# Optimization experiments

Hardware: AMD Instinct MI355X
Metric: run time of the kernel (lower is better)

The kernel has to match this reference:

```python
import jax, jax.numpy as jnp
import numpy as np

B, N, D = 2, 2048, 768
H = 12
DH = D // H
SCALE = DH ** -0.5


def setup_inputs() -> dict:
    key = jax.random.key(0)
    k1, k2, k3 = jax.random.split(key, 3)
    x = jax.random.normal(k1, (B, N, D), dtype=jnp.float32)
    w_qkv = jax.random.normal(k2, (D, 3 * D), dtype=jnp.float32) * (D ** -0.5)
    b_qkv = jnp.zeros((3 * D,), dtype=jnp.float32)
    w_proj = jax.random.normal(k3, (D, D), dtype=jnp.float32) * (D ** -0.5)
    b_proj = jnp.zeros((D,), dtype=jnp.float32)
    return {"x": x, "w_qkv": w_qkv, "b_qkv": b_qkv, "w_proj": w_proj, "b_proj": b_proj}


def reference(x, w_qkv, b_qkv, w_proj, b_proj):
    b, n, d = x.shape
    # qkv: (B, n, 3, H, DH) -> (3, B, H, n, DH)
    qkv = (x @ w_qkv + b_qkv).reshape(b, n, 3, H, DH).transpose(2, 0, 3, 1, 4)
    q, k, v = qkv[0], qkv[1], qkv[2]
    # naive full attention matrix (B, H, n, n)
    attn = jnp.einsum('bhqd,bhkd->bhqk', q, k) * SCALE
    attn = jax.nn.softmax(attn, axis=-1)
    out = jnp.einsum('bhqk,bhkd->bhqd', attn, v)  # (B, H, n, DH)
    out = out.transpose(0, 2, 1, 3).reshape(b, n, d)
    return out @ w_proj + b_proj
```

## Files before the change

kernel.cpp:

```cpp
#include <hip/hip_runtime.h>


#define CB 2
#define CN 2048
#define CD 768
#define CH 12
#define CDH 64
#define CEXPSCALE 0.18033688f

typedef __bf16 bf16x8 __attribute__((ext_vector_type(8)));
typedef float f32x4 __attribute__((ext_vector_type(4)));
typedef unsigned short u16x8 __attribute__((ext_vector_type(8)));

static __device__ __forceinline__ unsigned short f2bf(float f) {
  union { float f; unsigned u; } v; v.f = f;
  unsigned r = v.u + 0x7fffu + ((v.u >> 16) & 1u);
  return (unsigned short)(r >> 16);
}

static __device__ __forceinline__ void gld_lds16(const unsigned short* g, unsigned short* lds_base) {
  __builtin_amdgcn_global_load_lds(
      (const __attribute__((address_space(1))) unsigned int*)g,
      (__attribute__((address_space(3))) unsigned int*)(unsigned int)(unsigned long long)lds_base,
      16, 0, 0);
}

__global__ __launch_bounds__(256) void prep(const float* __restrict__ x,
                                            unsigned short* __restrict__ xb,
                                            const float* __restrict__ w_qkv,
                                            unsigned short* __restrict__ wqkv_t,
                                            const float* __restrict__ w_proj,
                                            unsigned short* __restrict__ wproj_t) {
  __shared__ __align__(16) unsigned short t[64][72];
  const int bid = blockIdx.x, tid = threadIdx.x;
#pragma unroll
  for (int it = 0; it < 2; ++it) {
    size_t i = ((size_t)(bid * 2 + it) * 256 + tid) * 8;
    f32x4 a = *(const f32x4*)&x[i];
    f32x4 b = *(const f32x4*)&x[i + 4];
    u16x8 o;
#pragma unroll
    for (int j = 0; j < 4; ++j) { o[j] = f2bf(a[j]); o[4 + j] = f2bf(b[j]); }
    *(u16x8*)&xb[i] = o;
  }
  if (bid >= 576) return;
  const float* src; unsigned short* dst; int R, C, c0, r0;
  if (bid < 432) { src = w_qkv; dst = wqkv_t; R = 768; C = 2304; c0 = (bid % 36) * 64; r0 = (bid / 36) * 64; }
  else { int u = bid - 432; src = w_proj; dst = wproj_t; R = 768; C = 768; c0 = (u % 12) * 64; r0 = (u / 12) * 64; }
#pragma unroll
  for (int i = 0; i < 4; ++i) {
    int c = tid + i * 256;
    int row = c >> 4, cc = (c & 15) * 4;
    f32x4 v = *(const f32x4*)&src[(size_t)(r0 + row) * C + c0 + cc];
#pragma unroll
    for (int j = 0; j < 4; ++j) t[row][cc + j] = f2bf(v[j]);
  }
  __syncthreads();
#pragma unroll
  for (int i = 0; i < 2; ++i) {
    int c = tid + i * 256;
    int drow = c >> 3, rc = (c & 7) * 8;
    u16x8 v;
#pragma unroll
    for (int j = 0; j < 8; ++j) v[j] = t[rc + j][drow];
    *(u16x8*)&dst[(size_t)(c0 + drow) * R + r0 + rc] = v;
  }
}

extern __shared__ __align__(16) unsigned short smem[];

template <int TM, int TN>
__global__ __launch_bounds__(256, 4) void gemm_db(const unsigned short* __restrict__ A,
                                                  const unsigned short* __restrict__ Bt,
                                                  const float* __restrict__ bias,
                                                  int M, int N, int K, int mode,
                                                  unsigned short* __restrict__ o0,
                                                  unsigned short* __restrict__ o1,
                                                  unsigned short* __restrict__ o2,
                                                  float* __restrict__ outF) {
  constexpr int NT = TN / 32;
  unsigned short* As = smem;
  unsigned short* Bs = smem + 2 * TM * 32;
  unsigned short* Ct = smem;
  const int tid = threadIdx.x;
  const int w = tid >> 6, lane = tid & 63, quad = lane >> 4, lc = lane & 15;
  const int wm = (w >> 1) * 32, wn = (w & 1) * (TN / 2);
  const int row0 = blockIdx.y * TM, col0 = blockIdx.x * TN;
  f32x4 acc[2][NT] = {};

  const int rl = lane >> 2, cl = lane & 3;
  const int gc = cl ^ ((rl >> 1) & 3);
  const int rsw = (lc >> 1) & 3;
  const int nk = K / 32;

  auto stage = [&](int kt, int buf) {
    const int k0 = kt * 32;
    gld_lds16(&A[(size_t)(row0 + w * 16 + rl) * K + k0 + gc * 8],
              &As[buf * (TM * 32) + (w * 16) * 32]);
#pragma unroll
    for (int jb = 0; jb < TN / 64; ++jb)
      gld_lds16(&Bt[(size_t)(col0 + w * (TN / 4) + jb * 16 + rl) * K + k0 + gc * 8],
                &Bs[buf * (TN * 32) + (w * (TN / 4) + jb * 16) * 32]);
  };

  stage(0, 0);
  for (int kt = 0; kt < nk; ++kt) {
    const int bb = kt & 1;
    __syncthreads();
    if (kt + 1 < nk) stage(kt + 1, bb ^ 1);
    bf16x8 af[2], bfv[NT];
#pragma unroll
    for (int mt = 0; mt < 2; ++mt)
      af[mt] = *(const bf16x8*)&As[bb * (TM * 32) + (wm + mt * 16 + lc) * 32 + (quad ^ rsw) * 8];
#pragma unroll
    for (int nt = 0; nt < NT; ++nt)
      bfv[nt] = *(const bf16x8*)&Bs[bb * (TN * 32) + (wn + nt * 16 + lc) * 32 + (quad ^ rsw) * 8];
#pragma unroll
    for (int mt = 0; mt < 2; ++mt)
#pragma unroll
      for (int nt = 0; nt < NT; ++nt)
        acc[mt][nt] = __builtin_amdgcn_mfma_f32_16x16x32_bf16(af[mt], bfv[nt], acc[mt][nt], 0, 0, 0);
  }

  if (mode == 0 && col0 >= 1536) {
    __syncthreads();
#pragma unroll
    for (int mt = 0; mt < 2; ++mt) {
#pragma unroll
      for (int nt = 0; nt < NT; ++nt) {
        int jl = wn + nt * 16 + lc;
        int il0 = wm + mt * 16 + quad * 4;
        float bj = bias[col0 + jl];
        unsigned short a0 = f2bf(acc[mt][nt][0] + bj);
        unsigned short a1 = f2bf(acc[mt][nt][1] + bj);
        unsigned short a2 = f2bf(acc[mt][nt][2] + bj);
        unsigned short a3 = f2bf(acc[mt][nt][3] + bj);
        uint2 dd;
        dd.x = (unsigned)a0 | ((unsigned)a1 << 16);
        dd.y = (unsigned)a2 | ((unsigned)a3 << 16);
        *(uint2*)&Ct[jl * (TM + 8) + il0] = dd;
      }
    }
    __syncthreads();
    const int b = row0 >> 11, n0 = row0 & 2047;
    constexpr int CPR = TM / 8;
#pragma unroll
    for (int i = 0; i < (TN * CPR) / 256; ++i) {
      int c = tid + i * 256;
      int jl = c / CPR, cc = (c % CPR) * 8;
      u16x8 v = *(const u16x8*)&Ct[jl * (TM + 8) + cc];
      int jcol = col0 - 1536 + jl;
      int h = jcol >> 6, d = jcol & 63;
      size_t gr = ((size_t)(b * CH + h) * CDH + d);
      *(u16x8*)&o2[gr * CN + n0 + cc] = v;
    }
  } else {
#pragma unroll
    for (int mt = 0; mt < 2; ++mt) {
#pragma unroll
      for (int nt = 0; nt < NT; ++nt) {
#pragma unroll
        for (int r = 0; r < 4; ++r) {
          int i = row0 + wm + mt * 16 + quad * 4 + r;
          int j = col0 + wn + nt * 16 + lc;
          float v = acc[mt][nt][r] + bias[j];
          if (mode == 0) {
            int b = i >> 11, n = i & 2047;
            int sec = (j >= 768) ? 1 : 0;
            int within = j - sec * 768;
            int h = within >> 6, d = within & 63;
            int bh = b * CH + h;
            if (sec == 0) o0[((size_t)bh * CN + n) * CDH + d] = f2bf(v * CEXPSCALE);
            else          o1[((size_t)bh * CN + n) * CDH + d] = f2bf(v);
          } else {
            outF[(size_t)i * N + j] = v;
          }
        }
      }
    }
  }
}

__global__ __launch_bounds__(256, 3) void attn64(const unsigned short* __restrict__ Q,
                                                 const unsigned short* __restrict__ K,
                                                 const unsigned short* __restrict__ Vt,
                                                 unsigned short* __restrict__ O) {
  __shared__ __align__(16) unsigned short Kls[2][64 * 64];
  __shared__ __align__(16) unsigned short Vls[2][64 * 64];
  __shared__ __align__(16) unsigned short P[4][16][88];
  const int bh = blockIdx.x, qt = blockIdx.y;
  const int tid = threadIdx.x;
  const int w = tid >> 6, lane = tid & 63, quad = lane >> 4, lc = lane & 15;
  const unsigned short* Qb = Q + (size_t)bh * CN * CDH;
  const unsigned short* Kb = K + (size_t)bh * CN * CDH;
  const unsigned short* Vb = Vt + (size_t)bh * CDH * CN;
  const int q0 = qt * 64 + w * 16;

  const int sr = lane >> 3, sc = lane & 7;
  const int sg = sc ^ sr;
  const int ksw = lc & 7;
  const int c0r = quad ^ ksw;
  const int c1r = c0r ^ 4;

  bf16x8 qf0 = *(const bf16x8*)&Qb[(size_t)(q0 + lc) * CDH + quad * 8];
  bf16x8 qf1 = *(const bf16x8*)&Qb[(size_t)(q0 + lc) * CDH + 32 + quad * 8];

  f32x4 o[4] = {};
  float rs = 0.f;

#pragma unroll
  for (int j2 = 0; j2 < 2; ++j2) {
    int j = w * 2 + j2;
    int r = j * 8 + sr;
    gld_lds16(&Kb[(size_t)r * CDH + sg * 8], &Kls[0][j * 8 * 64]);
    gld_lds16(&Vb[(size_t)r * CN + 0 + sg * 8], &Vls[0][j * 8 * 64]);
  }

  for (int kt = 0; kt < CN / 64; ++kt) {
    const int bb = kt & 1;
    __syncthreads();
    if (kt + 1 < CN / 64) {
      const int kn = (kt + 1) * 64;
#pragma unroll
      for (int j2 = 0; j2 < 2; ++j2) {
        int j = w * 2 + j2;
        int r = j * 8 + sr;
        gld_lds16(&Kb[(size_t)(kn + r) * CDH + sg * 8], &Kls[bb ^ 1][j * 8 * 64]);
        gld_lds16(&Vb[(size_t)r * CN + kn + sg * 8], &Vls[bb ^ 1][j * 8 * 64]);
      }
    }
#pragma unroll
    for (int t = 0; t < 4; ++t) {
      bf16x8 kf0 = *(const bf16x8*)&Kls[bb][(t * 16 + lc) * 64 + c0r * 8];
      bf16x8 kf1 = *(const bf16x8*)&Kls[bb][(t * 16 + lc) * 64 + c1r * 8];
      f32x4 z = {0.f, 0.f, 0.f, 0.f};
      z = __builtin_amdgcn_mfma_f32_16x16x32_bf16(kf0, qf0, z, 0, 0, 0);
      z = __builtin_amdgcn_mfma_f32_16x16x32_bf16(kf1, qf1, z, 0, 0, 0);
      float p0 = exp2f(z[0]);
      float p1 = exp2f(z[1]);
      float p2 = exp2f(z[2]);
      float p3 = exp2f(z[3]);
      rs += (p0 + p1) + (p2 + p3);
      unsigned d0 = __builtin_amdgcn_perm(__float_as_uint(p1), __float_as_uint(p0), 0x07060302u);
      unsigned d1 = __builtin_amdgcn_perm(__float_as_uint(p3), __float_as_uint(p2), 0x07060302u);
      uint2 dd; dd.x = d0; dd.y = d1;
      *(uint2*)&P[w][lc][t * 16 + quad * 4] = dd;
    }
    asm volatile("s_waitcnt lgkmcnt(0)" ::: "memory");
    bf16x8 pf0 = *(const bf16x8*)&P[w][lc][quad * 8];
    bf16x8 pf1 = *(const bf16x8*)&P[w][lc][32 + quad * 8];
#pragma unroll
    for (int dt = 0; dt < 4; ++dt) {
      bf16x8 vf0 = *(const bf16x8*)&Vls[bb][(dt * 16 + lc) * 64 + c0r * 8];
      bf16x8 vf1 = *(const bf16x8*)&Vls[bb][(dt * 16 + lc) * 64 + c1r * 8];
      o[dt] = __builtin_amdgcn_mfma_f32_16x16x32_bf16(pf0, vf0, o[dt], 0, 0, 0);
      o[dt] = __builtin_amdgcn_mfma_f32_16x16x32_bf16(pf1, vf1, o[dt], 0, 0, 0);
    }
  }

  rs += __shfl_xor(rs, 16, 64);
  rs += __shfl_xor(rs, 32, 64);
  const int b = bh / CH, h = bh - b * CH;
#pragma unroll
  for (int r = 0; r < 4; ++r) {
    float lr = __shfl(rs, quad * 4 + r, 64);
    float inv = 1.0f / lr;
#pragma unroll
    for (int dt = 0; dt < 4; ++dt) {
      int i = b * CN + q0 + quad * 4 + r;
      int j = h * CDH + dt * 16 + lc;
      O[(size_t)i * CD + j] = f2bf(o[dt][r] * inv);
    }
  }
}

extern "C" void kernel_launch(void* const* d_in, const int* in_sizes, int n_in,
                              void* d_out, int out_size, void* d_ws, size_t ws_size,
                              hipStream_t stream) {
  const float* x      = (const float*)d_in[0];
  const float* w_qkv  = (const float*)d_in[1];
  const float* b_qkv  = (const float*)d_in[2];
  const float* w_proj = (const float*)d_in[3];
  const float* b_proj = (const float*)d_in[4];
  float* out = (float*)d_out;
  unsigned short* ws = (unsigned short*)d_ws;

  unsigned short* xb      = ws;
  unsigned short* wqkv_t  = xb + (size_t)4096 * 768;
  unsigned short* wproj_t = wqkv_t + (size_t)2304 * 768;
  unsigned short* Qs  = wproj_t + (size_t)768 * 768;
  unsigned short* Ks  = Qs  + (size_t)CB * CH * CN * CDH;
  unsigned short* Vts = Ks  + (size_t)CB * CH * CN * CDH;
  unsigned short* AO  = Vts + (size_t)CB * CH * CN * CDH;

  const size_t smem_qkv  = (size_t)2 * (64 + 128) * 32 * 2;
  const size_t smem_proj = (size_t)2 * (64 + 64) * 32 * 2;

  prep<<<768, 256, 0, stream>>>(x, xb, w_qkv, wqkv_t, w_proj, wproj_t);
  gemm_db<64, 128><<<dim3(2304 / 128, 4096 / 64), 256, smem_qkv, stream>>>(
      xb, wqkv_t, b_qkv, 4096, 2304, 768, 0, Qs, Ks, Vts, nullptr);
  attn64<<<dim3(CB * CH, CN / 64), 256, 0, stream>>>(Qs, Ks, Vts, AO);
  gemm_db<64, 64><<<dim3(768 / 64, 4096 / 64), 256, smem_proj, stream>>>(
      AO, wproj_t, b_proj, 4096, 768, 768, 1, nullptr, nullptr, nullptr, out);
}
```

Baseline: 172.1 us.

## Split KV tile across wave pairs with 32-query register blocking in attention

Each wave now handles 32 queries against half of each 64-key tile instead of 16 queries against the whole tile. This reuses each K and V fragment loaded from LDS across two query sub-tiles, halving the per-wave LDS reads for K/V. Partial outputs and row sums are combined across wave pairs through shared memory at the end, which costs extra syncs and LDS traffic. It also adds s_setprio around the MFMA sections and uses a smaller padded P buffer.

New measurement: 168.0 us. 1.02x faster.

```diff
diff --git a/kernel.cpp b/kernel.cpp
--- a/kernel.cpp
+++ b/kernel.cpp
@@ -187,26 +187,34 @@
                                                  unsigned short* __restrict__ O) {
   __shared__ __align__(16) unsigned short Kls[2][64 * 64];
   __shared__ __align__(16) unsigned short Vls[2][64 * 64];
-  __shared__ __align__(16) unsigned short P[4][16][88];
-  const int bh = blockIdx.x, qt = blockIdx.y;
+  __shared__ __align__(16) unsigned short P[4][32 * 40];
+  __shared__ float rsb[2][2][2][16];
+  const int bh = blockIdx.x, qt0 = blockIdx.y;
   const int tid = threadIdx.x;
   const int w = tid >> 6, lane = tid & 63, quad = lane >> 4, lc = lane & 15;
+  const int qg = w & 1, kvh = w >> 1;
   const unsigned short* Qb = Q + (size_t)bh * CN * CDH;
   const unsigned short* Kb = K + (size_t)bh * CN * CDH;
   const unsigned short* Vb = Vt + (size_t)bh * CDH * CN;
-  const int q0 = qt * 64 + w * 16;
+  const int q0w = qt0 * 64 + qg * 32;
 
   const int sr = lane >> 3, sc = lane & 7;
   const int sg = sc ^ sr;
   const int ksw = lc & 7;
-  const int c0r = quad ^ ksw;
-  const int c1r = c0r ^ 4;
-
-  bf16x8 qf0 = *(const bf16x8*)&Qb[(size_t)(q0 + lc) * CDH + quad * 8];
-  bf16x8 qf1 = *(const bf16x8*)&Qb[(size_t)(q0 + lc) * CDH + 32 + quad * 8];
-
-  f32x4 o[4] = {};
-  float rs = 0.f;
+  const int c0 = (quad ^ ksw) * 8;
+  const int c1 = ((4 | quad) ^ ksw) * 8;
+  const int vch = (((kvh << 2) | quad) ^ ksw) * 8;
+  const int krow0 = kvh * 32;
+
+  bf16x8 qf[2][2];
+#pragma unroll
+  for (int qt = 0; qt < 2; ++qt)
+#pragma unroll
+    for (int hh = 0; hh < 2; ++hh)
+      qf[qt][hh] = *(const bf16x8*)&Qb[(size_t)(q0w + qt * 16 + lc) * CDH + hh * 32 + quad * 8];
+
+  f32x4 o[2][4] = {};
+  float rs0 = 0.f, rs1 = 0.f;
 
 #pragma unroll
   for (int j2 = 0; j2 < 2; ++j2) {
@@ -229,47 +237,83 @@
         gld_lds16(&Vb[(size_t)r * CN + kn + sg * 8], &Vls[bb ^ 1][j * 8 * 64]);
       }
     }
-#pragma unroll
-    for (int t = 0; t < 4; ++t) {
-      bf16x8 kf0 = *(const bf16x8*)&Kls[bb][(t * 16 + lc) * 64 + c0r * 8];
-      bf16x8 kf1 = *(const bf16x8*)&Kls[bb][(t * 16 + lc) * 64 + c1r * 8];
-      f32x4 z = {0.f, 0.f, 0.f, 0.f};
-      z = __builtin_amdgcn_mfma_f32_16x16x32_bf16(kf0, qf0, z, 0, 0, 0);
-      z = __builtin_amdgcn_mfma_f32_16x16x32_bf16(kf1, qf1, z, 0, 0, 0);
-      float p0 = exp2f(z[0]);
-      float p1 = exp2f(z[1]);
-      float p2 = exp2f(z[2]);
-      float p3 = exp2f(z[3]);
-      rs += (p0 + p1) + (p2 + p3);
-      unsigned d0 = __builtin_amdgcn_perm(__float_as_uint(p1), __float_as_uint(p0), 0x07060302u);
-      unsigned d1 = __builtin_amdgcn_perm(__float_as_uint(p3), __float_as_uint(p2), 0x07060302u);
-      uint2 dd; dd.x = d0; dd.y = d1;
-      *(uint2*)&P[w][lc][t * 16 + quad * 4] = dd;
-    }
+    bf16x8 kf[2][2];
+#pragma unroll
+    for (int kvt = 0; kvt < 2; ++kvt) {
+      const int row = (krow0 + kvt * 16 + lc) * 64;
+      kf[kvt][0] = *(const bf16x8*)&Kls[bb][row + c0];
+      kf[kvt][1] = *(const bf16x8*)&Kls[bb][row + c1];
+    }
+    f32x4 z[2][2] = {};
+    __builtin_amdgcn_s_setprio(1);
+#pragma unroll
+    for (int kvt = 0; kvt < 2; ++kvt)
+#pragma unroll
+      for (int qt = 0; qt < 2; ++qt) {
+        z[kvt][qt] = __builtin_amdgcn_mfma_f32_16x16x32_bf16(kf[kvt][0], qf[qt][0], z[kvt][qt], 0, 0, 0);
+        z[kvt][qt] = __builtin_amdgcn_mfma_f32_16x16x32_bf16(kf[kvt][1], qf[qt][1], z[kvt][qt], 0, 0, 0);
+      }
+    __builtin_amdgcn_s_setprio(0);
+#pragma unroll
+    for (int kvt = 0; kvt < 2; ++kvt)
+#pragma unroll
+      for (int qt = 0; qt < 2; ++qt) {
+        float p0 = exp2f(z[kvt][qt][0]);
+        float p1 = exp2f(z[kvt][qt][1]);
+        float p2 = exp2f(z[kvt][qt][2]);
+        float p3 = exp2f(z[kvt][qt][3]);
+        if (qt == 0) rs0 += (p0 + p1) + (p2 + p3);
+        else         rs1 += (p0 + p1) + (p2 + p3);
+        unsigned d0 = __builtin_amdgcn_perm(__float_as_uint(p1), __float_as_uint(p0), 0x07060302u);
+        unsigned d1 = __builtin_amdgcn_perm(__float_as_uint(p3), __float_as_uint(p2), 0x07060302u);
+        uint2 dd; dd.x = d0; dd.y = d1;
+        *(uint2*)&P[w][(qt * 16 + lc) * 40 + kvt * 16 + quad * 4] = dd;
+      }
     asm volatile("s_waitcnt lgkmcnt(0)" ::: "memory");
-    bf16x8 pf0 = *(const bf16x8*)&P[w][lc][quad * 8];
-    bf16x8 pf1 = *(const bf16x8*)&P[w][lc][32 + quad * 8];
+    bf16x8 pf0 = *(const bf16x8*)&P[w][(0 * 16 + lc) * 40 + quad * 8];
+    bf16x8 pf1 = *(const bf16x8*)&P[w][(1 * 16 + lc) * 40 + quad * 8];
+    __builtin_amdgcn_s_setprio(1);
 #pragma unroll
     for (int dt = 0; dt < 4; ++dt) {
-      bf16x8 vf0 = *(const bf16x8*)&Vls[bb][(dt * 16 + lc) * 64 + c0r * 8];
-      bf16x8 vf1 = *(const bf16x8*)&Vls[bb][(dt * 16 + lc) * 64 + c1r * 8];
-      o[dt] = __builtin_amdgcn_mfma_f32_16x16x32_bf16(pf0, vf0, o[dt], 0, 0, 0);
-      o[dt] = __builtin_amdgcn_mfma_f32_16x16x32_bf16(pf1, vf1, o[dt], 0, 0, 0);
-    }
-  }
-
-  rs += __shfl_xor(rs, 16, 64);
-  rs += __shfl_xor(rs, 32, 64);
-  const int b = bh / CH, h = bh - b * CH;
-#pragma unroll
-  for (int r = 0; r < 4; ++r) {
-    float lr = __shfl(rs, quad * 4 + r, 64);
-    float inv = 1.0f / lr;
-#pragma unroll
-    for (int dt = 0; dt < 4; ++dt) {
-      int i = b * CN + q0 + quad * 4 + r;
-      int j = h * CDH + dt * 16 + lc;
-      O[(size_t)i * CD + j] = f2bf(o[dt][r] * inv);
+      bf16x8 vf = *(const bf16x8*)&Vls[bb][(dt * 16 + lc) * 64 + vch];
+      o[0][dt] = __builtin_amdgcn_mfma_f32_16x16x32_bf16(pf0, vf, o[0][dt], 0, 0, 0);
+      o[1][dt] = __builtin_amdgcn_mfma_f32_16x16x32_bf16(pf1, vf, o[1][dt], 0, 0, 0);
+    }
+    __builtin_amdgcn_s_setprio(0);
+  }
+
+  rs0 += __shfl_xor(rs0, 16, 64); rs0 += __shfl_xor(rs0, 32, 64);
+  rs1 += __shfl_xor(rs1, 16, 64); rs1 += __shfl_xor(rs1, 32, 64);
+  if (lane < 16) { rsb[qg][kvh][0][lane] = rs0; rsb[qg][kvh][1][lane] = rs1; }
+  __syncthreads();
+  float* ob = (float*)&Kls[0][0];
+  if (kvh == 1) {
+#pragma unroll
+    for (int qt = 0; qt < 2; ++qt)
+#pragma unroll
+      for (int dt = 0; dt < 4; ++dt)
+        *(f32x4*)&ob[(qg * 8 + qt * 4 + dt) * 256 + lane * 4] = o[qt][dt];
+  }
+  __syncthreads();
+  if (kvh == 0) {
+    const int b = bh / CH, h = bh - b * CH;
+#pragma unroll
+    for (int qt = 0; qt < 2; ++qt) {
+#pragma unroll
+      for (int dt = 0; dt < 4; ++dt) {
+        f32x4 t = *(const f32x4*)&ob[(qg * 8 + qt * 4 + dt) * 256 + lane * 4];
+        o[qt][dt] += t;
+      }
+#pragma unroll
+      for (int r = 0; r < 4; ++r) {
+        float inv = 1.0f / (rsb[qg][0][qt][quad * 4 + r] + rsb[qg][1][qt][quad * 4 + r]);
+        int i = b * CN + q0w + qt * 16 + quad * 4 + r;
+#pragma unroll
+        for (int dt = 0; dt < 4; ++dt) {
+          int j = h * CDH + dt * 16 + lc;
+          O[(size_t)i * CD + j] = f2bf(o[qt][dt][r] * inv);
+        }
+      }
     }
   }
 }
```

## Keep attention probabilities in registers by permuting K row loads

Applied to the files above, without the earlier changes.

Loads K rows into shared memory in a permuted order so that the QK^T MFMA output layout lines up with the A-operand layout the PV MFMA expects. The probabilities can then be packed into bf16 registers directly, removing the per-warp P staging buffer in LDS along with its write, wait and read-back. It also batches the K/V fragment loads ahead of the MFMAs, brackets the MFMA groups with s_setprio, and raises the launch-bounds occupancy hint from 3 to 4. The cost is higher register pressure from holding all K/V fragments at once, and correctness depends on the permutation mapping being exact.

Result: faster. 168.2 us (-2.3%).

```diff
diff --git a/kernel.cpp b/kernel.cpp
--- a/kernel.cpp
+++ b/kernel.cpp
@@ -181,29 +181,37 @@
   }
 }
 
-__global__ __launch_bounds__(256, 3) void attn64(const unsigned short* __restrict__ Q,
+__global__ __launch_bounds__(256, 4) void attn64(const unsigned short* __restrict__ Q,
                                                  const unsigned short* __restrict__ K,
                                                  const unsigned short* __restrict__ Vt,
                                                  unsigned short* __restrict__ O) {
   __shared__ __align__(16) unsigned short Kls[2][64 * 64];
   __shared__ __align__(16) unsigned short Vls[2][64 * 64];
-  __shared__ __align__(16) unsigned short P[4][16][88];
-  const int bh = blockIdx.x, qt = blockIdx.y;
+  const int bh = blockIdx.x, qt0 = blockIdx.y;
   const int tid = threadIdx.x;
   const int w = tid >> 6, lane = tid & 63, quad = lane >> 4, lc = lane & 15;
   const unsigned short* Qb = Q + (size_t)bh * CN * CDH;
   const unsigned short* Kb = K + (size_t)bh * CN * CDH;
   const unsigned short* Vb = Vt + (size_t)bh * CDH * CN;
-  const int q0 = qt * 64 + w * 16;
+  const int q0w = qt0 * 64 + w * 16;
 
   const int sr = lane >> 3, sc = lane & 7;
   const int sg = sc ^ sr;
   const int ksw = lc & 7;
-  const int c0r = quad ^ ksw;
-  const int c1r = c0r ^ 4;
-
-  bf16x8 qf0 = *(const bf16x8*)&Qb[(size_t)(q0 + lc) * CDH + quad * 8];
-  bf16x8 qf1 = *(const bf16x8*)&Qb[(size_t)(q0 + lc) * CDH + 32 + quad * 8];
+  const int c0 = (quad ^ ksw) * 8;
+  const int c1 = ((4 | quad) ^ ksw) * 8;
+
+  int ks[2];
+#pragma unroll
+  for (int j2 = 0; j2 < 2; ++j2) {
+    int s = (w * 2 + j2) * 8 + sr;
+    ks[j2] = ((s & 28) << 1) | ((s & 32) >> 3) | (s & 3);
+  }
+
+  bf16x8 qf[2];
+#pragma unroll
+  for (int hh = 0; hh < 2; ++hh)
+    qf[hh] = *(const bf16x8*)&Qb[(size_t)(q0w + lc) * CDH + hh * 32 + quad * 8];
 
   f32x4 o[4] = {};
   float rs = 0.f;
@@ -212,7 +220,7 @@
   for (int j2 = 0; j2 < 2; ++j2) {
     int j = w * 2 + j2;
     int r = j * 8 + sr;
-    gld_lds16(&Kb[(size_t)r * CDH + sg * 8], &Kls[0][j * 8 * 64]);
+    gld_lds16(&Kb[(size_t)ks[j2] * CDH + sg * 8], &Kls[0][j * 8 * 64]);
     gld_lds16(&Vb[(size_t)r * CN + 0 + sg * 8], &Vls[0][j * 8 * 64]);
   }
 
@@ -225,37 +233,57 @@
       for (int j2 = 0; j2 < 2; ++j2) {
         int j = w * 2 + j2;
         int r = j * 8 + sr;
-        gld_lds16(&Kb[(size_t)(kn + r) * CDH + sg * 8], &Kls[bb ^ 1][j * 8 * 64]);
+        gld_lds16(&Kb[(size_t)(kn + ks[j2]) * CDH + sg * 8], &Kls[bb ^ 1][j * 8 * 64]);
         gld_lds16(&Vb[(size_t)r * CN + kn + sg * 8], &Vls[bb ^ 1][j * 8 * 64]);
       }
     }
-#pragma unroll
-    for (int t = 0; t < 4; ++t) {
-      bf16x8 kf0 = *(const bf16x8*)&Kls[bb][(t * 16 + lc) * 64 + c0r * 8];
-      bf16x8 kf1 = *(const bf16x8*)&Kls[bb][(t * 16 + lc) * 64 + c1r * 8];
-      f32x4 z = {0.f, 0.f, 0.f, 0.f};
-      z = __builtin_amdgcn_mfma_f32_16x16x32_bf16(kf0, qf0, z, 0, 0, 0);
-      z = __builtin_amdgcn_mfma_f32_16x16x32_bf16(kf1, qf1, z, 0, 0, 0);
-      float p0 = exp2f(z[0]);
-      float p1 = exp2f(z[1]);
-      float p2 = exp2f(z[2]);
-      float p3 = exp2f(z[3]);
-      rs += (p0 + p1) + (p2 + p3);
-      unsigned d0 = __builtin_amdgcn_perm(__float_as_uint(p1), __float_as_uint(p0), 0x07060302u);
-      unsigned d1 = __builtin_amdgcn_perm(__float_as_uint(p3), __float_as_uint(p2), 0x07060302u);
-      uint2 dd; dd.x = d0; dd.y = d1;
-      *(uint2*)&P[w][lc][t * 16 + quad * 4] = dd;
-    }
-    asm volatile("s_waitcnt lgkmcnt(0)" ::: "memory");
-    bf16x8 pf0 = *(const bf16x8*)&P[w][lc][quad * 8];
-    bf16x8 pf1 = *(const bf16x8*)&P[w][lc][32 + quad * 8];
+    bf16x8 kf[4][2];
+#pragma unroll
+    for (int kvt = 0; kvt < 4; ++kvt) {
+      const int row = (kvt * 16 + lc) * 64;
+      kf[kvt][0] = *(const bf16x8*)&Kls[bb][row + c0];
+      kf[kvt][1] = *(const bf16x8*)&Kls[bb][row + c1];
+    }
+    bf16x8 vf[4][2];
 #pragma unroll
     for (int dt = 0; dt < 4; ++dt) {
-      bf16x8 vf0 = *(const bf16x8*)&Vls[bb][(dt * 16 + lc) * 64 + c0r * 8];
-      bf16x8 vf1 = *(const bf16x8*)&Vls[bb][(dt * 16 + lc) * 64 + c1r * 8];
-      o[dt] = __builtin_amdgcn_mfma_f32_16x16x32_bf16(pf0, vf0, o[dt], 0, 0, 0);
-      o[dt] = __builtin_amdgcn_mfma_f32_16x16x32_bf16(pf1, vf1, o[dt], 0, 0, 0);
-    }
+      const int row = (dt * 16 + lc) * 64;
+      vf[dt][0] = *(const bf16x8*)&Vls[bb][row + c0];
+      vf[dt][1] = *(const bf16x8*)&Vls[bb][row + c1];
+    }
+    f32x4 z[4] = {};
+    __builtin_amdgcn_s_setprio(1);
+#pragma unroll
+    for (int kvt = 0; kvt < 4; ++kvt) {
+      z[kvt] = __builtin_amdgcn_mfma_f32_16x16x32_bf16(kf[kvt][0], qf[0], z[kvt], 0, 0, 0);
+      z[kvt] = __builtin_amdgcn_mfma_f32_16x16x32_bf16(kf[kvt][1], qf[1], z[kvt], 0, 0, 0);
+    }
+    __builtin_amdgcn_s_setprio(0);
+    union PU { unsigned u[4]; bf16x8 v; } P0, P1;
+#pragma unroll
+    for (int g = 0; g < 2; ++g) {
+      unsigned pu[4];
+#pragma unroll
+      for (int hpair = 0; hpair < 2; ++hpair) {
+        const int kvt = hpair * 2 + g;
+        float e0 = exp2f(z[kvt][0]);
+        float e1 = exp2f(z[kvt][1]);
+        float e2 = exp2f(z[kvt][2]);
+        float e3 = exp2f(z[kvt][3]);
+        rs += (e0 + e1) + (e2 + e3);
+        pu[hpair * 2]     = __builtin_amdgcn_perm(__float_as_uint(e1), __float_as_uint(e0), 0x07060302u);
+        pu[hpair * 2 + 1] = __builtin_amdgcn_perm(__float_as_uint(e3), __float_as_uint(e2), 0x07060302u);
+      }
+      if (g == 0) { P0.u[0] = pu[0]; P0.u[1] = pu[1]; P0.u[2] = pu[2]; P0.u[3] = pu[3]; }
+      else        { P1.u[0] = pu[0]; P1.u[1] = pu[1]; P1.u[2] = pu[2]; P1.u[3] = pu[3]; }
+    }
+    __builtin_amdgcn_s_setprio(1);
+#pragma unroll
+    for (int dt = 0; dt < 4; ++dt) {
+      o[dt] = __builtin_amdgcn_mfma_f32_16x16x32_bf16(P0.v, vf[dt][0], o[dt], 0, 0, 0);
+      o[dt] = __builtin_amdgcn_mfma_f32_16x16x32_bf16(P1.v, vf[dt][1], o[dt], 0, 0, 0);
+    }
+    __builtin_amdgcn_s_setprio(0);
   }
 
   rs += __shfl_xor(rs, 16, 64);
@@ -265,9 +293,9 @@
   for (int r = 0; r < 4; ++r) {
     float lr = __shfl(rs, quad * 4 + r, 64);
     float inv = 1.0f / lr;
+    int i = b * CN + q0w + quad * 4 + r;
 #pragma unroll
     for (int dt = 0; dt < 4; ++dt) {
-      int i = b * CN + q0 + quad * 4 + r;
       int j = h * CDH + dt * 16 + lc;
       O[(size_t)i * CD + j] = f2bf(o[dt][r] * inv);
     }
```
